# Kernel tuning notes

Hardware: AMD Instinct MI355X
Metric: run time of the kernel (lower is better)

The kernel has to match this reference:

```python
import jax, jax.numpy as jnp
import numpy as np

N = 100000   # nodes
E = 1600000  # edges
F_IN = 64    # n_features
H = 32       # hidden_size
OUT = 1      # output_size


def _lin(k, fan_in, fan_out):
    return (jax.random.normal(k, (fan_in, fan_out), jnp.float32) / np.sqrt(fan_in)).astype(jnp.float32)


def setup_inputs() -> dict:
    key = jax.random.key(0)
    ks = jax.random.split(key, 16)
    x = jax.random.normal(ks[0], (N, F_IN), jnp.float32)
    edge_index = jax.random.randint(ks[1], (2, E), 0, N, dtype=jnp.int64)
    # guarantee current_node (=0) has outgoing edges so the legal-move mask is non-empty
    edge_index = edge_index.at[0, :64].set(0)
    edge_attr = jax.random.uniform(ks[2], (E,), jnp.float32)
    return {
        "x": x, "edge_index": edge_index, "edge_attr": edge_attr, "current_node": 0,
        # conv_in: GraphConv(F_IN -> H)
        "Win_rel": _lin(ks[3], F_IN, H), "bin_rel": jnp.zeros((H,), jnp.float32), "Win_root": _lin(ks[4], F_IN, H),
        # conv_hidden: GraphConv(H -> H)
        "Wh_rel": _lin(ks[5], H, H), "bh_rel": jnp.zeros((H,), jnp.float32), "Wh_root": _lin(ks[6], H, H),
        # policy_conv: GraphConv(H -> OUT)
        "Wp_rel": _lin(ks[7], H, OUT), "bp_rel": jnp.zeros((OUT,), jnp.float32), "Wp_root": _lin(ks[8], H, OUT),
        # value_conv: GraphConv(H -> OUT)
        "Wv_rel": _lin(ks[9], H, OUT), "bv_rel": jnp.zeros((OUT,), jnp.float32), "Wv_root": _lin(ks[10], H, OUT),
    }


def _graph_conv(h, src, dst, ew, W_rel, b_rel, W_root):
    # PyG GraphConv: out_i = W_root h_i + W_rel * sum_{j->i} e_ji * h_j + b
    msg = h[src] * ew[:, None]                              # [E, d] gather + scale
    agg = jax.ops.segment_sum(msg, dst, num_segments=N)      # [N, d] scatter-add
    return agg @ W_rel + b_rel + h @ W_root


def reference(x, edge_index, edge_attr, current_node,
              Win_rel, bin_rel, Win_root,
              Wh_rel, bh_rel, Wh_root,
              Wp_rel, bp_rel, Wp_root,
              Wv_rel, bv_rel, Wv_root):
    src, dst = edge_index[0], edge_index[1]
    h = jax.nn.relu(_graph_conv(x, src, dst, edge_attr, Win_rel, bin_rel, Win_root))
    h = jax.nn.relu(_graph_conv(h, src, dst, edge_attr, Wh_rel, bh_rel, Wh_root))
    p = _graph_conv(h, src, dst, edge_attr, Wp_rel, bp_rel, Wp_root)  # [N, 1]
    v = _graph_conv(h, src, dst, edge_attr, Wv_rel, bv_rel, Wv_root)  # [N, 1]
    # illegal_moves_mask: 1 for nodes directly reachable from current_node
    hit = (src == current_node).astype(jnp.float32)
    mask = (jnp.zeros((N,), jnp.float32).at[dst].add(hit) > 0).astype(jnp.float32)
    p_m = mask * p.T                                   # [1, N]
    p_m = jnp.where(p_m == 0, -jnp.inf, p_m)
    p_soft = jax.nn.softmax(p_m, axis=1)
    v_m = mask * v.T                                   # [1, N]
    return p_soft.reshape(-1), v_m.reshape(-1)
```

## Files before the change

kernel.cpp:

```cpp
#include <hip/hip_runtime.h>
#include <hip/hip_fp16.h>
#include <cmath>

static constexpr int NN = 100000;
static constexpr int NE = 1600000;
static const size_t NW = (size_t)NN * 32;
static constexpr int SUB = 256;
static constexpr int NSUB = 391;
static constexpr int CH = 4096;
static constexpr int NCH = (NE + CH - 1) / CH;
static constexpr int BCAP = 5200;
static constexpr int CSRN = NSUB * BCAP;
static constexpr int MCAP = 4096;

__device__ __forceinline__ float ent_w(unsigned e)
{
    return __half2float(__ushort_as_half((unsigned short)(e >> 17)));
}
__device__ __forceinline__ int ent_s(unsigned e)
{
    int s = (int)(e & 0x1FFFF);
    return s < NN ? s : NN - 1;
}

__device__ __forceinline__ float4 pack8(const float* v)
{
    union { __half2 h2[4]; float4 f4; } u;
    u.h2[0] = __floats2half2_rn(v[0], v[1]);
    u.h2[1] = __floats2half2_rn(v[2], v[3]);
    u.h2[2] = __floats2half2_rn(v[4], v[5]);
    u.h2[3] = __floats2half2_rn(v[6], v[7]);
    return u.f4;
}

__global__ void __launch_bounds__(512) fused_build_mm1_k(
    const int* __restrict__ src, const int* __restrict__ dst,
    const float* __restrict__ ew, const int* __restrict__ curp,
    int* __restrict__ maskb, int* __restrict__ mcount, int* __restrict__ mlist,
    int* __restrict__ bcnt, uint2* __restrict__ buckets,
    const float* __restrict__ x, const float* __restrict__ Wrel,
    const float* __restrict__ Wroot, const float* __restrict__ bin,
    __half* __restrict__ proj1, __half* __restrict__ root1)
{
    __shared__ union {
        struct {
            uint2 sBuf[CH];
            int lhist[NSUB];
            int lpos[NSUB];
            int lstart[NSUB];
            int lbase[NSUB];
            int tscan[512];
        } s;
        struct {
            float sX[128 * 65];
            float sW[64 * 68];
        } m;
    } u;

    int t = threadIdx.x;
    int bid = blockIdx.x;

    if (bid < NCH) {
        for (int i = t; i < NSUB; i += 512) { u.s.lhist[i] = 0; u.s.lpos[i] = 0; }
        __syncthreads();
        int c0 = bid * CH;
        int cur = curp[0];
        uint2 rent[CH / 512];
        int rb[CH / 512];
#pragma unroll
        for (int it = 0; it < CH / 512; ++it) {
            int e = c0 + it * 512 + t;
            rb[it] = -1;
            if (e < NE) {
                int d = dst[e];
                int sv = src[e];
                if ((unsigned)d < (unsigned)NN) {
                    rb[it] = d >> 8;
                    unsigned bits = __half_as_ushort(__float2half(ew[e]));
                    rent[it].x = ((unsigned)sv & 0x1FFFF) | (bits << 17);
                    rent[it].y = (unsigned)d;
                    atomicAdd(&u.s.lhist[rb[it]], 1);
                    if (sv == cur) {
                        if (atomicExch(maskb + d, 1) == 0) {
                            int idx = atomicAdd(mcount, 1);
                            if (idx < MCAP) mlist[idx] = d;
                        }
                    }
                }
            }
        }
        __syncthreads();
        int v = (t < NSUB) ? u.s.lhist[t] : 0;
        u.s.tscan[t] = v;
        __syncthreads();
        for (int sh = 1; sh < 512; sh <<= 1) {
            int xv = u.s.tscan[t];
            int a = (t >= sh) ? u.s.tscan[t - sh] : 0;
            __syncthreads();
            u.s.tscan[t] = xv + a;
            __syncthreads();
        }
        if (t < NSUB) {
            u.s.lstart[t] = u.s.tscan[t] - v;
            u.s.lbase[t] = (v > 0) ? atomicAdd(&bcnt[t], v) : 0;
        }
        __syncthreads();
#pragma unroll
        for (int it = 0; it < CH / 512; ++it) {
            if (rb[it] >= 0) {
                int p = atomicAdd(&u.s.lpos[rb[it]], 1);
                u.s.sBuf[u.s.lstart[rb[it]] + p] = rent[it];
            }
        }
        __syncthreads();
        int total = u.s.lstart[NSUB - 1] + u.s.lhist[NSUB - 1];
        for (int j = t; j < total; j += 512) {
            uint2 en = u.s.sBuf[j];
            int b = (int)(en.y >> 8);
            if (b >= NSUB) b = NSUB - 1;
            unsigned pos = (unsigned)(u.s.lbase[b] + (j - u.s.lstart[b]));
            if (pos < (unsigned)BCAP) buckets[(size_t)b * BCAP + pos] = en;
        }
    } else {
        int mb = bid - NCH;
        for (int i = t; i < 64 * 32; i += 512) {
            int k = i >> 5, j = i & 31;
            u.m.sW[k * 68 + j] = Wrel[i];
            u.m.sW[k * 68 + 32 + j] = Wroot[i];
        }
        int base = mb * 128;
        for (int i = t; i < 2048; i += 512) {
            int node = i >> 4;
            int k = (i & 15) * 4;
            int n = base + node;
            if (n >= NN) n = NN - 1;
            float4 v4 = *(const float4*)(x + (size_t)n * 64 + k);
            float* p = u.m.sX + node * 65 + k;
            p[0] = v4.x; p[1] = v4.y; p[2] = v4.z; p[3] = v4.w;
        }
        __syncthreads();
        int cg = t & 7;
        int ng = t >> 3;
        int c0m = 8 * cg;
        float acc[2][8] = {};
        for (int k = 0; k < 64; ++k) {
            float xv0 = u.m.sX[(2 * ng + 0) * 65 + k];
            float xv1 = u.m.sX[(2 * ng + 1) * 65 + k];
            float4 w0 = *(const float4*)(u.m.sW + k * 68 + c0m);
            float4 w1 = *(const float4*)(u.m.sW + k * 68 + c0m + 4);
            const float* wp = (const float*)&w0;
#pragma unroll
            for (int j = 0; j < 4; ++j) {
                float w = wp[j];
                acc[0][j] = fmaf(xv0, w, acc[0][j]);
                acc[1][j] = fmaf(xv1, w, acc[1][j]);
            }
            const float* wq = (const float*)&w1;
#pragma unroll
            for (int j = 0; j < 4; ++j) {
                float w = wq[j];
                acc[0][4 + j] = fmaf(xv0, w, acc[0][4 + j]);
                acc[1][4 + j] = fmaf(xv1, w, acc[1][4 + j]);
            }
        }
#pragma unroll
        for (int r = 0; r < 2; ++r) {
            int n = base + 2 * ng + r;
            if (n >= NN) break;
            if (cg < 4) {
                *(float4*)(proj1 + (size_t)n * 32 + c0m) = pack8(acc[r]);
            } else {
                int c = c0m - 32;
                float vv[8];
#pragma unroll
                for (int j = 0; j < 8; ++j) vv[j] = acc[r][j] + bin[c + j];
                *(float4*)(root1 + (size_t)n * 32 + c) = pack8(vv);
            }
        }
    }
}

__global__ void __launch_bounds__(512) sortB_k(
    const uint2* __restrict__ buckets, const int* __restrict__ bcnt,
    unsigned* __restrict__ csr4, int* __restrict__ deg, int* __restrict__ off)
{
    __shared__ uint2 sBuf[BCAP];
    __shared__ int lhist[SUB];
    __shared__ int lstart[SUB];
    __shared__ int lcur[SUB];
    __shared__ int tscan[256];
    int g = blockIdx.x, t = threadIdx.x;
    if (t < SUB) { lhist[t] = 0; lcur[t] = 0; }
    __syncthreads();
    int cnt = bcnt[g];
    if (cnt < 0) cnt = 0;
    if (cnt > BCAP) cnt = BCAP;
    const uint2* bk = buckets + (size_t)g * BCAP;
    for (int i = t; i < cnt; i += 512) {
        uint2 e = bk[i];
        sBuf[i] = e;
        atomicAdd(&lhist[e.y & (SUB - 1)], 1);
    }
    __syncthreads();
    if (t < 256) tscan[t] = lhist[t];
    __syncthreads();
    for (int s = 1; s < 256; s <<= 1) {
        int x = 0, a = 0;
        if (t < 256) { x = tscan[t]; a = (t >= s) ? tscan[t - s] : 0; }
        __syncthreads();
        if (t < 256) tscan[t] = x + a;
        __syncthreads();
    }
    if (t < 256) lstart[t] = tscan[t] - lhist[t];
    __syncthreads();
    int base = g * BCAP;
    for (int i = t; i < cnt; i += 512) {
        uint2 e = sBuf[i];
        int ld = (int)(e.y & (SUB - 1));
        int p = atomicAdd(&lcur[ld], 1);
        unsigned pos = (unsigned)(base + lstart[ld] + p);
        if (pos < (unsigned)CSRN) csr4[pos] = e.x;
    }
    if (t < SUB) {
        int n = g * SUB + t;
        if (n < NN) {
            deg[n] = lhist[t];
            off[n] = base + lstart[t];
        }
    }
}

__global__ void __launch_bounds__(256) mm2_k(
    const __half* __restrict__ h1, const float* __restrict__ Wrel,
    const float* __restrict__ Wroot, const float* __restrict__ bh,
    __half* __restrict__ proj2, __half* __restrict__ root2)
{
    __shared__ float sX[128 * 33];
    __shared__ float sW[32 * 68];
    int t = threadIdx.x;
    for (int i = t; i < 32 * 32; i += 256) {
        int k = i >> 5, j = i & 31;
        sW[k * 68 + j] = Wrel[i];
        sW[k * 68 + 32 + j] = Wroot[i];
    }
    int base = blockIdx.x * 128;
    for (int i = t; i < 512; i += 256) {
        int node = i >> 2;
        int hs = (i & 3) * 8;
        int n = base + node;
        if (n >= NN) n = NN - 1;
        float4 v = *(const float4*)(h1 + (size_t)n * 32 + hs);
        const __half2* hp = (const __half2*)&v;
        float* p = sX + node * 33 + hs;
#pragma unroll
        for (int u = 0; u < 4; ++u) {
            float2 f2 = __half22float2(hp[u]);
            p[2 * u] = f2.x;
            p[2 * u + 1] = f2.y;
        }
    }
    __syncthreads();
    int cg = t & 7;
    int ng = t >> 3;
    int c0 = 8 * cg;
    float acc[4][8] = {};
    for (int k = 0; k < 32; ++k) {
        float xv0 = sX[(4 * ng + 0) * 33 + k];
        float xv1 = sX[(4 * ng + 1) * 33 + k];
        float xv2 = sX[(4 * ng + 2) * 33 + k];
        float xv3 = sX[(4 * ng + 3) * 33 + k];
        float4 w0 = *(const float4*)(sW + k * 68 + c0);
        float4 w1 = *(const float4*)(sW + k * 68 + c0 + 4);
        const float* wp = (const float*)&w0;
#pragma unroll
        for (int j = 0; j < 4; ++j) {
            float w = wp[j];
            acc[0][j] = fmaf(xv0, w, acc[0][j]);
            acc[1][j] = fmaf(xv1, w, acc[1][j]);
            acc[2][j] = fmaf(xv2, w, acc[2][j]);
            acc[3][j] = fmaf(xv3, w, acc[3][j]);
        }
        const float* wq = (const float*)&w1;
#pragma unroll
        for (int j = 0; j < 4; ++j) {
            float w = wq[j];
            acc[0][4 + j] = fmaf(xv0, w, acc[0][4 + j]);
            acc[1][4 + j] = fmaf(xv1, w, acc[1][4 + j]);
            acc[2][4 + j] = fmaf(xv2, w, acc[2][4 + j]);
            acc[3][4 + j] = fmaf(xv3, w, acc[3][4 + j]);
        }
    }
#pragma unroll
    for (int r = 0; r < 4; ++r) {
        int n = base + 4 * ng + r;
        if (n >= NN) break;
        if (cg < 4) {
            *(float4*)(proj2 + (size_t)n * 32 + c0) = pack8(acc[r]);
        } else {
            int c = c0 - 32;
            float v[8];
#pragma unroll
            for (int j = 0; j < 8; ++j) v[j] = acc[r][j] + bh[c + j];
            *(float4*)(root2 + (size_t)n * 32 + c) = pack8(v);
        }
    }
}

__global__ void __launch_bounds__(256) agg1_v4(
    const __half* __restrict__ proj1, const __half* __restrict__ root1,
    const unsigned* __restrict__ csr4, const int* __restrict__ off,
    const int* __restrict__ deg, __half* __restrict__ h1)
{
    int t = threadIdx.x;
    int q = t & 3;
    int f0 = q * 8;
    int n = blockIdx.x * 64 + (t >> 2);
    if (n >= NN) return;
    int st = off[n];
    int dg = deg[n];
    if (st < 0) st = 0;
    if (st > CSRN) st = CSRN;
    if (dg < 0) dg = 0;
    if (dg > CSRN - st) dg = CSRN - st;
    float acc[8] = {0.f, 0.f, 0.f, 0.f, 0.f, 0.f, 0.f, 0.f};
    int i = 0;
    for (; i + 3 < dg; i += 4) {
        unsigned e0 = csr4[st + i];
        unsigned e1 = csr4[st + i + 1];
        unsigned e2 = csr4[st + i + 2];
        unsigned e3 = csr4[st + i + 3];
        float4 r0 = *(const float4*)(proj1 + (size_t)ent_s(e0) * 32 + f0);
        float4 r1 = *(const float4*)(proj1 + (size_t)ent_s(e1) * 32 + f0);
        float4 r2 = *(const float4*)(proj1 + (size_t)ent_s(e2) * 32 + f0);
        float4 r3 = *(const float4*)(proj1 + (size_t)ent_s(e3) * 32 + f0);
        float w0 = ent_w(e0), w1 = ent_w(e1), w2 = ent_w(e2), w3 = ent_w(e3);
        const __half2* h0 = (const __half2*)&r0;
        const __half2* h1p = (const __half2*)&r1;
        const __half2* h2p = (const __half2*)&r2;
        const __half2* h3p = (const __half2*)&r3;
#pragma unroll
        for (int u = 0; u < 4; ++u) {
            float2 a = __half22float2(h0[u]);
            float2 b = __half22float2(h1p[u]);
            float2 c = __half22float2(h2p[u]);
            float2 d = __half22float2(h3p[u]);
            acc[2 * u]     = fmaf(w0, a.x, acc[2 * u]);
            acc[2 * u + 1] = fmaf(w0, a.y, acc[2 * u + 1]);
            acc[2 * u]     = fmaf(w1, b.x, acc[2 * u]);
            acc[2 * u + 1] = fmaf(w1, b.y, acc[2 * u + 1]);
            acc[2 * u]     = fmaf(w2, c.x, acc[2 * u]);
            acc[2 * u + 1] = fmaf(w2, c.y, acc[2 * u + 1]);
            acc[2 * u]     = fmaf(w3, d.x, acc[2 * u]);
            acc[2 * u + 1] = fmaf(w3, d.y, acc[2 * u + 1]);
        }
    }
    for (; i < dg; ++i) {
        unsigned e0 = csr4[st + i];
        float w0 = ent_w(e0);
        float4 r0 = *(const float4*)(proj1 + (size_t)ent_s(e0) * 32 + f0);
        const __half2* h0 = (const __half2*)&r0;
#pragma unroll
        for (int u = 0; u < 4; ++u) {
            float2 a = __half22float2(h0[u]);
            acc[2 * u] = fmaf(w0, a.x, acc[2 * u]);
            acc[2 * u + 1] = fmaf(w0, a.y, acc[2 * u + 1]);
        }
    }
    float4 rr = *(const float4*)(root1 + (size_t)n * 32 + f0);
    const __half2* rp = (const __half2*)&rr;
    float h[8];
#pragma unroll
    for (int u = 0; u < 4; ++u) {
        float2 f2 = __half22float2(rp[u]);
        h[2 * u] = fmaxf(acc[2 * u] + f2.x, 0.f);
        h[2 * u + 1] = fmaxf(acc[2 * u + 1] + f2.y, 0.f);
    }
    *(float4*)(h1 + (size_t)n * 32 + f0) = pack8(h);
}

__global__ void __launch_bounds__(256) agg2_v4(
    const __half* __restrict__ proj2, const __half* __restrict__ root2,
    const float* __restrict__ Wp_rel, const float* __restrict__ Wp_root,
    const float* __restrict__ bp, const float* __restrict__ Wv_rel,
    const float* __restrict__ Wv_root, const float* __restrict__ bv,
    const unsigned* __restrict__ csr4, const int* __restrict__ off,
    const int* __restrict__ deg, float2* __restrict__ pv,
    float* __restrict__ pbase, float* __restrict__ vbase,
    float* __restrict__ out_p, float* __restrict__ out_v)
{
    __shared__ float sHead[4 * 32];
    if (threadIdx.x < 32) {
        sHead[threadIdx.x] = Wp_rel[threadIdx.x];
        sHead[32 + threadIdx.x] = Wp_root[threadIdx.x];
        sHead[64 + threadIdx.x] = Wv_rel[threadIdx.x];
        sHead[96 + threadIdx.x] = Wv_root[threadIdx.x];
    }
    __syncthreads();
    int t = threadIdx.x;
    int q = t & 3;
    int f0 = q * 8;
    int n = blockIdx.x * 64 + (t >> 2);
    if (n >= NN) return;
    int st = off[n];
    int dg = deg[n];
    if (st < 0) st = 0;
    if (st > CSRN) st = CSRN;
    if (dg < 0) dg = 0;
    if (dg > CSRN - st) dg = CSRN - st;
    float acc[8] = {0.f, 0.f, 0.f, 0.f, 0.f, 0.f, 0.f, 0.f};
    int i = 0;
    for (; i + 3 < dg; i += 4) {
        unsigned e0 = csr4[st + i];
        unsigned e1 = csr4[st + i + 1];
        unsigned e2 = csr4[st + i + 2];
        unsigned e3 = csr4[st + i + 3];
        float4 r0 = *(const float4*)(proj2 + (size_t)ent_s(e0) * 32 + f0);
        float4 r1 = *(const float4*)(proj2 + (size_t)ent_s(e1) * 32 + f0);
        float4 r2 = *(const float4*)(proj2 + (size_t)ent_s(e2) * 32 + f0);
        float4 r3 = *(const float4*)(proj2 + (size_t)ent_s(e3) * 32 + f0);
        float w0 = ent_w(e0), w1 = ent_w(e1), w2 = ent_w(e2), w3 = ent_w(e3);
        const __half2* h0 = (const __half2*)&r0;
        const __half2* h1p = (const __half2*)&r1;
        const __half2* h2p = (const __half2*)&r2;
        const __half2* h3p = (const __half2*)&r3;
#pragma unroll
        for (int u = 0; u < 4; ++u) {
            float2 a = __half22float2(h0[u]);
            float2 b = __half22float2(h1p[u]);
            float2 c = __half22float2(h2p[u]);
            float2 d = __half22float2(h3p[u]);
            acc[2 * u]     = fmaf(w0, a.x, acc[2 * u]);
            acc[2 * u + 1] = fmaf(w0, a.y, acc[2 * u + 1]);
            acc[2 * u]     = fmaf(w1, b.x, acc[2 * u]);
            acc[2 * u + 1] = fmaf(w1, b.y, acc[2 * u + 1]);
            acc[2 * u]     = fmaf(w2, c.x, acc[2 * u]);
            acc[2 * u + 1] = fmaf(w2, c.y, acc[2 * u + 1]);
            acc[2 * u]     = fmaf(w3, d.x, acc[2 * u]);
            acc[2 * u + 1] = fmaf(w3, d.y, acc[2 * u + 1]);
        }
    }
    for (; i < dg; ++i) {
        unsigned e0 = csr4[st + i];
        float w0 = ent_w(e0);
        float4 r0 = *(const float4*)(proj2 + (size_t)ent_s(e0) * 32 + f0);
        const __half2* h0 = (const __half2*)&r0;
#pragma unroll
        for (int u = 0; u < 4; ++u) {
            float2 a = __half22float2(h0[u]);
            acc[2 * u] = fmaf(w0, a.x, acc[2 * u]);
            acc[2 * u + 1] = fmaf(w0, a.y, acc[2 * u + 1]);
        }
    }
    float4 rr = *(const float4*)(root2 + (size_t)n * 32 + f0);
    const __half2* rp = (const __half2*)&rr;
    float h[8];
#pragma unroll
    for (int u = 0; u < 4; ++u) {
        float2 f2 = __half22float2(rp[u]);
        h[2 * u] = fmaxf(acc[2 * u] + f2.x, 0.f);
        h[2 * u + 1] = fmaxf(acc[2 * u + 1] + f2.y, 0.f);
    }
    float prv = 0.f, pov = 0.f, vrv = 0.f, vov = 0.f;
#pragma unroll
    for (int j = 0; j < 8; ++j) {
        prv = fmaf(h[j], sHead[f0 + j], prv);
        pov = fmaf(h[j], sHead[32 + f0 + j], pov);
        vrv = fmaf(h[j], sHead[64 + f0 + j], vrv);
        vov = fmaf(h[j], sHead[96 + f0 + j], vov);
    }
#pragma unroll
    for (int m = 1; m <= 2; m <<= 1) {
        prv += __shfl_xor(prv, m, 64);
        pov += __shfl_xor(pov, m, 64);
        vrv += __shfl_xor(vrv, m, 64);
        vov += __shfl_xor(vov, m, 64);
    }
    if (q == 0) {
        pv[n] = make_float2(prv, vrv);
        pbase[n] = pov + bp[0];
        vbase[n] = vov + bv[0];
        out_p[n] = 0.f;
        out_v[n] = 0.f;
    }
}

__global__ void __launch_bounds__(256) masked_softmax_k(
    const int* __restrict__ mlist, const int* __restrict__ mcount,
    const unsigned* __restrict__ csr4, const int* __restrict__ off,
    const int* __restrict__ deg, const float2* __restrict__ pv,
    const float* __restrict__ pbase, const float* __restrict__ vbase,
    float* __restrict__ out_p, float* __restrict__ out_v)
{
    __shared__ float sPm[MCAP];
    __shared__ float sV[MCAP];
    __shared__ int sN[MCAP];
    __shared__ float sMx, sSum;
    __shared__ float sred[4];
    int m = mcount[0];
    if (m > MCAP) m = MCAP;
    if (m < 0) m = 0;
    for (int idx = threadIdx.x; idx < m; idx += 256) {
        int n = mlist[idx];
        if ((unsigned)n >= (unsigned)NN) n = 0;
        sN[idx] = n;
        int st = off[n];
        int dg = deg[n];
        if (st < 0) st = 0;
        if (st > CSRN) st = CSRN;
        if (dg < 0) dg = 0;
        if (dg > CSRN - st) dg = CSRN - st;
        float pa = 0.f, va = 0.f;
        for (int i = 0; i < dg; ++i) {
            unsigned ent = csr4[st + i];
            int s = ent_s(ent);
            float w = ent_w(ent);
            float2 tv = pv[s];
            pa = fmaf(tv.x, w, pa);
            va = fmaf(tv.y, w, va);
        }
        float p = pa + pbase[n];
        sPm[idx] = (p == 0.f) ? -INFINITY : p;
        sV[idx] = va + vbase[n];
    }
    __syncthreads();
    float mx = -INFINITY;
    for (int i = threadIdx.x; i < m; i += 256) mx = fmaxf(mx, sPm[i]);
#pragma unroll
    for (int k = 32; k; k >>= 1) mx = fmaxf(mx, __shfl_xor(mx, k, 64));
    if ((threadIdx.x & 63) == 0) sred[threadIdx.x >> 6] = mx;
    __syncthreads();
    if (threadIdx.x == 0)
        sMx = fmaxf(fmaxf(sred[0], sred[1]), fmaxf(sred[2], sred[3]));
    __syncthreads();
    float sum = 0.f;
    for (int i = threadIdx.x; i < m; i += 256) {
        float x = sPm[i];
        sum += (x == -INFINITY) ? 0.f : expf(x - sMx);
    }
#pragma unroll
    for (int k = 32; k; k >>= 1) sum += __shfl_xor(sum, k, 64);
    if ((threadIdx.x & 63) == 0) sred[threadIdx.x >> 6] = sum;
    __syncthreads();
    if (threadIdx.x == 0) sSum = sred[0] + sred[1] + sred[2] + sred[3];
    __syncthreads();
    for (int idx = threadIdx.x; idx < m; idx += 256) {
        int n = sN[idx];
        float x = sPm[idx];
        out_p[n] = (x == -INFINITY) ? 0.f : expf(x - sMx) / sSum;
        out_v[n] = sV[idx];
    }
}

extern "C" void kernel_launch(void* const* d_in, const int* in_sizes, int n_in,
                              void* d_out, int out_size, void* d_ws,
                              size_t ws_size, hipStream_t stream)
{
    const float* x        = (const float*)d_in[0];
    const int*   ei       = (const int*)d_in[1];
    const float* ew       = (const float*)d_in[2];
    const int*   cur      = (const int*)d_in[3];
    const float* Win_rel  = (const float*)d_in[4];
    const float* bin_rel  = (const float*)d_in[5];
    const float* Win_root = (const float*)d_in[6];
    const float* Wh_rel   = (const float*)d_in[7];
    const float* bh_rel   = (const float*)d_in[8];
    const float* Wh_root  = (const float*)d_in[9];
    const float* Wp_rel   = (const float*)d_in[10];
    const float* bp       = (const float*)d_in[11];
    const float* Wp_root  = (const float*)d_in[12];
    const float* Wv_rel   = (const float*)d_in[13];
    const float* bv       = (const float*)d_in[14];
    const float* Wv_root  = (const float*)d_in[15];

    const int* srcA = ei;
    const int* dstA = ei + NE;

    char* w8 = (char*)d_ws;
    unsigned* csr4 = (unsigned*)w8;
    int* deg    = (int*)(csr4 + CSRN);
    int* off    = deg + NN;
    int* maskb  = off + NN;
    int* mcount = maskb + NN;
    int* bcnt   = mcount + 8;
    int* mlist  = bcnt + 400;
    __half* proj1 = (__half*)(mlist + MCAP);
    __half* root1 = proj1 + NW;
    __half* h1    = root1 + NW;
    __half* proj2 = h1 + NW;
    __half* root2 = proj2 + NW;
    float2* pv    = (float2*)(root2 + NW);
    float* pbase  = (float*)(pv + NN);
    float* vbase  = pbase + NN;
    uint2* buckets = (uint2*)(vbase + NN);

    float* out_p = (float*)d_out;
    float* out_v = out_p + NN;

    const int NB_MM    = (NN + 127) / 128;
    const int NB_AGG   = (NN + 63) / 64;
    const int NB_FUSED = NCH + NB_MM;

    hipMemsetAsync(maskb, 0, ((size_t)NN + 8 + 400) * sizeof(int), stream);

    fused_build_mm1_k<<<NB_FUSED, 512, 0, stream>>>(
        srcA, dstA, ew, cur, maskb, mcount, mlist, bcnt, buckets,
        x, Win_rel, Win_root, bin_rel, proj1, root1);
    sortB_k<<<NSUB, 512, 0, stream>>>(buckets, bcnt, csr4, deg, off);

    agg1_v4<<<NB_AGG, 256, 0, stream>>>(proj1, root1, csr4, off, deg, h1);
    mm2_k<<<NB_MM, 256, 0, stream>>>(h1, Wh_rel, Wh_root, bh_rel, proj2, root2);
    agg2_v4<<<NB_AGG, 256, 0, stream>>>(proj2, root2, Wp_rel, Wp_root, bp,
                                        Wv_rel, Wv_root, bv, csr4, off, deg,
                                        pv, pbase, vbase, out_p, out_v);
    masked_softmax_k<<<1, 256, 0, stream>>>(mlist, mcount, csr4, off, deg, pv,
                                            pbase, vbase, out_p, out_v);
}
```

Before: 252.9 us.

## Fuse layer-1 aggregation with hidden matmul and shrink bucket entry format

```diff
diff --git a/kernel.cpp b/kernel.cpp
--- a/kernel.cpp
+++ b/kernel.cpp
@@ -7,7 +7,7 @@
 static const size_t NW = (size_t)NN * 32;
 static constexpr int SUB = 256;
 static constexpr int NSUB = 391;
-static constexpr int CH = 4096;
+static constexpr int CH = 8192;
 static constexpr int NCH = (NE + CH - 1) / CH;
 static constexpr int BCAP = 5200;
 static constexpr int CSRN = NSUB * BCAP;
@@ -37,14 +37,16 @@
     const int* __restrict__ src, const int* __restrict__ dst,
     const float* __restrict__ ew, const int* __restrict__ curp,
     int* __restrict__ maskb, int* __restrict__ mcount, int* __restrict__ mlist,
-    int* __restrict__ bcnt, uint2* __restrict__ buckets,
+    int* __restrict__ bcnt, unsigned* __restrict__ bx,
+    unsigned char* __restrict__ bd,
     const float* __restrict__ x, const float* __restrict__ Wrel,
     const float* __restrict__ Wroot, const float* __restrict__ bin,
     __half* __restrict__ proj1, __half* __restrict__ root1)
 {
     __shared__ union {
         struct {
-            uint2 sBuf[CH];
+            unsigned sBufX[CH];
+            unsigned char sBufD[CH];
             int lhist[NSUB];
             int lpos[NSUB];
             int lstart[NSUB];
@@ -65,22 +67,13 @@
         __syncthreads();
         int c0 = bid * CH;
         int cur = curp[0];
-        uint2 rent[CH / 512];
-        int rb[CH / 512];
-#pragma unroll
         for (int it = 0; it < CH / 512; ++it) {
             int e = c0 + it * 512 + t;
-            rb[it] = -1;
             if (e < NE) {
                 int d = dst[e];
-                int sv = src[e];
                 if ((unsigned)d < (unsigned)NN) {
-                    rb[it] = d >> 8;
-                    unsigned bits = __half_as_ushort(__float2half(ew[e]));
-                    rent[it].x = ((unsigned)sv & 0x1FFFF) | (bits << 17);
-                    rent[it].y = (unsigned)d;
-                    atomicAdd(&u.s.lhist[rb[it]], 1);
-                    if (sv == cur) {
+                    atomicAdd(&u.s.lhist[d >> 8], 1);
+                    if (src[e] == cur) {
                         if (atomicExch(maskb + d, 1) == 0) {
                             int idx = atomicAdd(mcount, 1);
                             if (idx < MCAP) mlist[idx] = d;
@@ -105,21 +98,34 @@
             u.s.lbase[t] = (v > 0) ? atomicAdd(&bcnt[t], v) : 0;
         }
         __syncthreads();
-#pragma unroll
         for (int it = 0; it < CH / 512; ++it) {
-            if (rb[it] >= 0) {
-                int p = atomicAdd(&u.s.lpos[rb[it]], 1);
-                u.s.sBuf[u.s.lstart[rb[it]] + p] = rent[it];
-            }
-        }
-        __syncthreads();
-        int total = u.s.lstart[NSUB - 1] + u.s.lhist[NSUB - 1];
-        for (int j = t; j < total; j += 512) {
-            uint2 en = u.s.sBuf[j];
-            int b = (int)(en.y >> 8);
-            if (b >= NSUB) b = NSUB - 1;
-            unsigned pos = (unsigned)(u.s.lbase[b] + (j - u.s.lstart[b]));
-            if (pos < (unsigned)BCAP) buckets[(size_t)b * BCAP + pos] = en;
+            int e = c0 + it * 512 + t;
+            if (e < NE) {
+                int d = dst[e];
+                if ((unsigned)d < (unsigned)NN) {
+                    int b = d >> 8;
+                    int p = atomicAdd(&u.s.lpos[b], 1);
+                    int pos = u.s.lstart[b] + p;
+                    unsigned bits = __half_as_ushort(__float2half(ew[e]));
+                    u.s.sBufX[pos] = ((unsigned)src[e] & 0x1FFFF) | (bits << 17);
+                    u.s.sBufD[pos] = (unsigned char)(d & 255);
+                }
+            }
+        }
+        __syncthreads();
+        int wid = t >> 6, lane = t & 63;
+        for (int b = wid; b < NSUB; b += 8) {
+            int s0 = u.s.lstart[b];
+            int cb = u.s.lhist[b];
+            int gb = u.s.lbase[b];
+            size_t base = (size_t)b * BCAP;
+            for (int j = lane; j < cb; j += 64) {
+                unsigned pos = (unsigned)(gb + j);
+                if (pos < (unsigned)BCAP) {
+                    bx[base + pos] = u.s.sBufX[s0 + j];
+                    bd[base + pos] = u.s.sBufD[s0 + j];
+                }
+            }
         }
     } else {
         int mb = bid - NCH;
@@ -181,10 +187,12 @@
 }
 
 __global__ void __launch_bounds__(512) sortB_k(
-    const uint2* __restrict__ buckets, const int* __restrict__ bcnt,
+    const unsigned* __restrict__ bx, const unsigned char* __restrict__ bd,
+    const int* __restrict__ bcnt,
     unsigned* __restrict__ csr4, int* __restrict__ deg, int* __restrict__ off)
 {
-    __shared__ uint2 sBuf[BCAP];
+    __shared__ unsigned sX[BCAP];
+    __shared__ unsigned char sD[BCAP];
     __shared__ int lhist[SUB];
     __shared__ int lstart[SUB];
     __shared__ int lcur[SUB];
@@ -195,11 +203,13 @@
     int cnt = bcnt[g];
     if (cnt < 0) cnt = 0;
     if (cnt > BCAP) cnt = BCAP;
-    const uint2* bk = buckets + (size_t)g * BCAP;
+    size_t gbase = (size_t)g * BCAP;
     for (int i = t; i < cnt; i += 512) {
-        uint2 e = bk[i];
-        sBuf[i] = e;
-        atomicAdd(&lhist[e.y & (SUB - 1)], 1);
+        unsigned e = bx[gbase + i];
+        unsigned char d = bd[gbase + i];
+        sX[i] = e;
+        sD[i] = d;
+        atomicAdd(&lhist[d], 1);
     }
     __syncthreads();
     if (t < 256) tscan[t] = lhist[t];
@@ -215,11 +225,10 @@
     __syncthreads();
     int base = g * BCAP;
     for (int i = t; i < cnt; i += 512) {
-        uint2 e = sBuf[i];
-        int ld = (int)(e.y & (SUB - 1));
+        int ld = (int)sD[i];
         int p = atomicAdd(&lcur[ld], 1);
         unsigned pos = (unsigned)(base + lstart[ld] + p);
-        if (pos < (unsigned)CSRN) csr4[pos] = e.x;
+        if (pos < (unsigned)CSRN) csr4[pos] = sX[i];
     }
     if (t < SUB) {
         int n = g * SUB + t;
@@ -230,12 +239,15 @@
     }
 }
 
-__global__ void __launch_bounds__(256) mm2_k(
-    const __half* __restrict__ h1, const float* __restrict__ Wrel,
-    const float* __restrict__ Wroot, const float* __restrict__ bh,
+__global__ void __launch_bounds__(256) agg1_mm2_k(
+    const __half* __restrict__ proj1, const __half* __restrict__ root1,
+    const unsigned* __restrict__ csr4, const int* __restrict__ off,
+    const int* __restrict__ deg,
+    const float* __restrict__ Wrel, const float* __restrict__ Wroot,
+    const float* __restrict__ bh,
     __half* __restrict__ proj2, __half* __restrict__ root2)
 {
-    __shared__ float sX[128 * 33];
+    __shared__ float sX[64 * 33];
     __shared__ float sW[32 * 68];
     int t = threadIdx.x;
     for (int i = t; i < 32 * 32; i += 256) {
@@ -243,139 +255,112 @@
         sW[k * 68 + j] = Wrel[i];
         sW[k * 68 + 32 + j] = Wroot[i];
     }
-    int base = blockIdx.x * 128;
-    for (int i = t; i < 512; i += 256) {
-        int node = i >> 2;
-        int hs = (i & 3) * 8;
-        int n = base + node;
-        if (n >= NN) n = NN - 1;
-        float4 v = *(const float4*)(h1 + (size_t)n * 32 + hs);
-        const __half2* hp = (const __half2*)&v;
-        float* p = sX + node * 33 + hs;
+    int q = t & 3;
+    int f0 = q * 8;
+    int l = t >> 2;
+    int n = blockIdx.x * 64 + l;
+    bool active = n < NN;
+    float h[8] = {};
+    if (active) {
+        int st = off[n];
+        int dg = deg[n];
+        if (st < 0) st = 0;
+        if (st > CSRN) st = CSRN;
+        if (dg < 0) dg = 0;
+        if (dg > CSRN - st) dg = CSRN - st;
+        float acc[8] = {0.f, 0.f, 0.f, 0.f, 0.f, 0.f, 0.f, 0.f};
+        int i = 0;
+        for (; i + 3 < dg; i += 4) {
+            unsigned e0 = csr4[st + i];
+            unsigned e1 = csr4[st + i + 1];
+            unsigned e2 = csr4[st + i + 2];
+            unsigned e3 = csr4[st + i + 3];
+            float4 r0 = *(const float4*)(proj1 + (size_t)ent_s(e0) * 32 + f0);
+            float4 r1 = *(const float4*)(proj1 + (size_t)ent_s(e1) * 32 + f0);
+            float4 r2 = *(const float4*)(proj1 + (size_t)ent_s(e2) * 32 + f0);
+            float4 r3 = *(const float4*)(proj1 + (size_t)ent_s(e3) * 32 + f0);
+            float w0 = ent_w(e0), w1 = ent_w(e1), w2 = ent_w(e2), w3 = ent_w(e3);
+            const __half2* h0 = (const __half2*)&r0;
+            const __half2* h1p = (const __half2*)&r1;
+            const __half2* h2p = (const __half2*)&r2;
+            const __half2* h3p = (const __half2*)&r3;
+#pragma unroll
+            for (int u = 0; u < 4; ++u) {
+                float2 a = __half22float2(h0[u]);
+                float2 b = __half22float2(h1p[u]);
+                float2 c = __half22float2(h2p[u]);
+                float2 d = __half22float2(h3p[u]);
+                acc[2 * u]     = fmaf(w0, a.x, acc[2 * u]);
+                acc[2 * u + 1] = fmaf(w0, a.y, acc[2 * u + 1]);
+                acc[2 * u]     = fmaf(w1, b.x, acc[2 * u]);
+                acc[2 * u + 1] = fmaf(w1, b.y, acc[2 * u + 1]);
+                acc[2 * u]     = fmaf(w2, c.x, acc[2 * u]);
+                acc[2 * u + 1] = fmaf(w2, c.y, acc[2 * u + 1]);
+                acc[2 * u]     = fmaf(w3, d.x, acc[2 * u]);
+                acc[2 * u + 1] = fmaf(w3, d.y, acc[2 * u + 1]);
+            }
+        }
+        for (; i < dg; ++i) {
+            unsigned e0 = csr4[st + i];
+            float w0 = ent_w(e0);
+            float4 r0 = *(const float4*)(proj1 + (size_t)ent_s(e0) * 32 + f0);
+            const __half2* h0 = (const __half2*)&r0;
+#pragma unroll
+            for (int u = 0; u < 4; ++u) {
+                float2 a = __half22float2(h0[u]);
+                acc[2 * u] = fmaf(w0, a.x, acc[2 * u]);
+                acc[2 * u + 1] = fmaf(w0, a.y, acc[2 * u + 1]);
+            }
+        }
+        float4 rr = *(const float4*)(root1 + (size_t)n * 32 + f0);
+        const __half2* rp = (const __half2*)&rr;
 #pragma unroll
         for (int u = 0; u < 4; ++u) {
-            float2 f2 = __half22float2(hp[u]);
-            p[2 * u] = f2.x;
-            p[2 * u + 1] = f2.y;
-        }
-    }
-    __syncthreads();
-    int cg = t & 7;
-    int ng = t >> 3;
-    int c0 = 8 * cg;
-    float acc[4][8] = {};
+            float2 f2 = __half22float2(rp[u]);
+            h[2 * u] = fmaxf(acc[2 * u] + f2.x, 0.f);
+            h[2 * u + 1] = fmaxf(acc[2 * u + 1] + f2.y, 0.f);
+        }
+    }
+#pragma unroll
+    for (int j = 0; j < 8; ++j) sX[l * 33 + f0 + j] = h[j];
+    __syncthreads();
+    int cg = t & 7, ng = t >> 3, c0 = 8 * cg;
+    int nb = blockIdx.x * 64;
+    float a2[2][8] = {};
     for (int k = 0; k < 32; ++k) {
-        float xv0 = sX[(4 * ng + 0) * 33 + k];
-        float xv1 = sX[(4 * ng + 1) * 33 + k];
-        float xv2 = sX[(4 * ng + 2) * 33 + k];
-        float xv3 = sX[(4 * ng + 3) * 33 + k];
+        float x0 = sX[(2 * ng + 0) * 33 + k];
+        float x1 = sX[(2 * ng + 1) * 33 + k];
         float4 w0 = *(const float4*)(sW + k * 68 + c0);
         float4 w1 = *(const float4*)(sW + k * 68 + c0 + 4);
         const float* wp = (const float*)&w0;
 #pragma unroll
         for (int j = 0; j < 4; ++j) {
             float w = wp[j];
-            acc[0][j] = fmaf(xv0, w, acc[0][j]);
-            acc[1][j] = fmaf(xv1, w, acc[1][j]);
-            acc[2][j] = fmaf(xv2, w, acc[2][j]);
-            acc[3][j] = fmaf(xv3, w, acc[3][j]);
+            a2[0][j] = fmaf(x0, w, a2[0][j]);
+            a2[1][j] = fmaf(x1, w, a2[1][j]);
         }
         const float* wq = (const float*)&w1;
 #pragma unroll
         for (int j = 0; j < 4; ++j) {
             float w = wq[j];
-            acc[0][4 + j] = fmaf(xv0, w, acc[0][4 + j]);
-            acc[1][4 + j] = fmaf(xv1, w, acc[1][4 + j]);
-            acc[2][4 + j] = fmaf(xv2, w, acc[2][4 + j]);
-            acc[3][4 + j] = fmaf(xv3, w, acc[3][4 + j]);
-        }
-    }
-#pragma unroll
-    for (int r = 0; r < 4; ++r) {
-        int n = base + 4 * ng + r;
-        if (n >= NN) break;
+            a2[0][4 + j] = fmaf(x0, w, a2[0][4 + j]);
+            a2[1][4 + j] = fmaf(x1, w, a2[1][4 + j]);
+        }
+    }
+#pragma unroll
+    for (int r = 0; r < 2; ++r) {
+        int n2 = nb + 2 * ng + r;
+        if (n2 >= NN) break;
         if (cg < 4) {
-            *(float4*)(proj2 + (size_t)n * 32 + c0) = pack8(acc[r]);
+            *(float4*)(proj2 + (size_t)n2 * 32 + c0) = pack8(a2[r]);
         } else {
             int c = c0 - 32;
-            float v[8];
-#pragma unroll
-            for (int j = 0; j < 8; ++j) v[j] = acc[r][j] + bh[c + j];
-            *(float4*)(root2 + (size_t)n * 32 + c) = pack8(v);
-        }
-    }
-}
-
-__global__ void __launch_bounds__(256) agg1_v4(
-    const __half* __restrict__ proj1, const __half* __restrict__ root1,
-    const unsigned* __restrict__ csr4, const int* __restrict__ off,
-    const int* __restrict__ deg, __half* __restrict__ h1)
-{
-    int t = threadIdx.x;
-    int q = t & 3;
-    int f0 = q * 8;
-    int n = blockIdx.x * 64 + (t >> 2);
-    if (n >= NN) return;
-    int st = off[n];
-    int dg = deg[n];
-    if (st < 0) st = 0;
-    if (st > CSRN) st = CSRN;
-    if (dg < 0) dg = 0;
-    if (dg > CSRN - st) dg = CSRN - st;
-    float acc[8] = {0.f, 0.f, 0.f, 0.f, 0.f, 0.f, 0.f, 0.f};
-    int i = 0;
-    for (; i + 3 < dg; i += 4) {
-        unsigned e0 = csr4[st + i];
-        unsigned e1 = csr4[st + i + 1];
-        unsigned e2 = csr4[st + i + 2];
-        unsigned e3 = csr4[st + i + 3];
-        float4 r0 = *(const float4*)(proj1 + (size_t)ent_s(e0) * 32 + f0);
-        float4 r1 = *(const float4*)(proj1 + (size_t)ent_s(e1) * 32 + f0);
-        float4 r2 = *(const float4*)(proj1 + (size_t)ent_s(e2) * 32 + f0);
-        float4 r3 = *(const float4*)(proj1 + (size_t)ent_s(e3) * 32 + f0);
-        float w0 = ent_w(e0), w1 = ent_w(e1), w2 = ent_w(e2), w3 = ent_w(e3);
-        const __half2* h0 = (const __half2*)&r0;
-        const __half2* h1p = (const __half2*)&r1;
-        const __half2* h2p = (const __half2*)&r2;
-        const __half2* h3p = (const __half2*)&r3;
-#pragma unroll
-        for (int u = 0; u < 4; ++u) {
-            float2 a = __half22float2(h0[u]);
-            float2 b = __half22float2(h1p[u]);
-            float2 c = __half22float2(h2p[u]);
-            float2 d = __half22float2(h3p[u]);
-            acc[2 * u]     = fmaf(w0, a.x, acc[2 * u]);
-            acc[2 * u + 1] = fmaf(w0, a.y, acc[2 * u + 1]);
-            acc[2 * u]     = fmaf(w1, b.x, acc[2 * u]);
-            acc[2 * u + 1] = fmaf(w1, b.y, acc[2 * u + 1]);
-            acc[2 * u]     = fmaf(w2, c.x, acc[2 * u]);
-            acc[2 * u + 1] = fmaf(w2, c.y, acc[2 * u + 1]);
-            acc[2 * u]     = fmaf(w3, d.x, acc[2 * u]);
-            acc[2 * u + 1] = fmaf(w3, d.y, acc[2 * u + 1]);
-        }
-    }
-    for (; i < dg; ++i) {
-        unsigned e0 = csr4[st + i];
-        float w0 = ent_w(e0);
-        float4 r0 = *(const float4*)(proj1 + (size_t)ent_s(e0) * 32 + f0);
-        const __half2* h0 = (const __half2*)&r0;
-#pragma unroll
-        for (int u = 0; u < 4; ++u) {
-            float2 a = __half22float2(h0[u]);
-            acc[2 * u] = fmaf(w0, a.x, acc[2 * u]);
-            acc[2 * u + 1] = fmaf(w0, a.y, acc[2 * u + 1]);
-        }
-    }
-    float4 rr = *(const float4*)(root1 + (size_t)n * 32 + f0);
-    const __half2* rp = (const __half2*)&rr;
-    float h[8];
-#pragma unroll
-    for (int u = 0; u < 4; ++u) {
-        float2 f2 = __half22float2(rp[u]);
-        h[2 * u] = fmaxf(acc[2 * u] + f2.x, 0.f);
-        h[2 * u + 1] = fmaxf(acc[2 * u + 1] + f2.y, 0.f);
-    }
-    *(float4*)(h1 + (size_t)n * 32 + f0) = pack8(h);
+            float vv[8];
+#pragma unroll
+            for (int j = 0; j < 8; ++j) vv[j] = a2[r][j] + bh[c + j];
+            *(float4*)(root2 + (size_t)n2 * 32 + c) = pack8(vv);
+        }
+    }
 }
 
 __global__ void __launch_bounds__(256) agg2_v4(
@@ -585,13 +570,13 @@
     int* mlist  = bcnt + 400;
     __half* proj1 = (__half*)(mlist + MCAP);
     __half* root1 = proj1 + NW;
-    __half* h1    = root1 + NW;
-    __half* proj2 = h1 + NW;
+    __half* proj2 = root1 + NW;
     __half* root2 = proj2 + NW;
     float2* pv    = (float2*)(root2 + NW);
     float* pbase  = (float*)(pv + NN);
     float* vbase  = pbase + NN;
-    uint2* buckets = (uint2*)(vbase + NN);
+    unsigned* bucket_x = (unsigned*)(vbase + NN);
+    unsigned char* bucket_d = (unsigned char*)(bucket_x + CSRN);
 
     float* out_p = (float*)d_out;
     float* out_v = out_p + NN;
@@ -603,12 +588,13 @@
     hipMemsetAsync(maskb, 0, ((size_t)NN + 8 + 400) * sizeof(int), stream);
 
     fused_build_mm1_k<<<NB_FUSED, 512, 0, stream>>>(
-        srcA, dstA, ew, cur, maskb, mcount, mlist, bcnt, buckets,
+        srcA, dstA, ew, cur, maskb, mcount, mlist, bcnt, bucket_x, bucket_d,
         x, Win_rel, Win_root, bin_rel, proj1, root1);
-    sortB_k<<<NSUB, 512, 0, stream>>>(buckets, bcnt, csr4, deg, off);
-
-    agg1_v4<<<NB_AGG, 256, 0, stream>>>(proj1, root1, csr4, off, deg, h1);
-    mm2_k<<<NB_MM, 256, 0, stream>>>(h1, Wh_rel, Wh_root, bh_rel, proj2, root2);
+    sortB_k<<<NSUB, 512, 0, stream>>>(bucket_x, bucket_d, bcnt, csr4, deg, off);
+
+    agg1_mm2_k<<<NB_AGG, 256, 0, stream>>>(proj1, root1, csr4, off, deg,
+                                           Wh_rel, Wh_root, bh_rel,
+                                           proj2, root2);
     agg2_v4<<<NB_AGG, 256, 0, stream>>>(proj2, root2, Wp_rel, Wp_root, bp,
                                         Wv_rel, Wv_root, bv, csr4, off, deg,
                                         pv, pbase, vbase, out_p, out_v);
```

After: 272.9 us. 7.9% more time.
